# Kernel tuning notes

Measured on AMD Instinct MI355X. Metric: run time of the kernel, lower is better.

Reference implementation:

```python
import jax, jax.numpy as jnp
import numpy as np
from jax import lax

N, T, D, W, H, V = 256, 64, 1280, 256, 512, 10000
NULL_IDX = 0  # ignore_index


def setup_inputs() -> dict:
    key = jax.random.key(0)
    ks = jax.random.split(key, 9)
    features = jax.random.normal(ks[0], (N, D), dtype=jnp.float32)
    captions = jax.random.randint(ks[1], (N, T + 1), 0, V, dtype=jnp.int64)
    # learned parameters
    W_proj = jax.random.normal(ks[2], (D, H), dtype=jnp.float32) / np.sqrt(D)
    b_proj = jnp.zeros((H,), dtype=jnp.float32)
    W_embed = jax.random.normal(ks[3], (V, W), dtype=jnp.float32) / np.sqrt(V)
    Wx = jax.random.normal(ks[4], (W, H), dtype=jnp.float32) / np.sqrt(W)
    Wh = jax.random.normal(ks[5], (H, H), dtype=jnp.float32) / np.sqrt(H)
    b = jnp.zeros((H,), dtype=jnp.float32)
    W_out = jax.random.normal(ks[6], (H, V), dtype=jnp.float32) / np.sqrt(H)
    b_out = jnp.zeros((V,), dtype=jnp.float32)
    return {"features": features, "captions": captions, "W_proj": W_proj,
            "b_proj": b_proj, "W_embed": W_embed, "Wx": Wx, "Wh": Wh, "b": b,
            "W_out": W_out, "b_out": b_out}


def reference(features, captions, W_proj, b_proj, W_embed, Wx, Wh, b, W_out, b_out):
    captions_in = captions[:, :-1]   # (N, T)
    captions_out = captions[:, 1:]   # (N, T)

    h0 = features @ W_proj + b_proj                      # (N, H)
    x = W_embed[captions_in]                             # (N, T, W)
    # Precompute input-to-hidden part; recurrence only needs h @ Wh.
    xWxb = jnp.einsum('ntw,wh->nth', x, Wx) + b          # (N, T, H)

    def step(h_prev, xt):
        h_next = jnp.tanh(h_prev @ Wh + xt)
        return h_next, h_next

    _, hs = lax.scan(step, h0, jnp.swapaxes(xWxb, 0, 1))  # (T, N, H)
    h = jnp.swapaxes(hs, 0, 1)                            # (N, T, H)

    scores = jnp.einsum('nth,hv->ntv', h, W_out) + b_out  # (N, T, V)
    logp = jax.nn.log_softmax(scores, axis=-1)
    nll = -jnp.take_along_axis(logp, captions_out[..., None], axis=-1)[..., 0]
    mask = (captions_out != NULL_IDX).astype(nll.dtype)
    loss = jnp.sum(nll * mask) / N
    return loss
```

## Files before the change

kernel.cpp:

```cpp
#include <hip/hip_runtime.h>
#include <hip/hip_bf16.h>
#include <hip/hip_fp8.h>

#define NB 256
#define TT 64
#define DD 1280
#define WW 256
#define HH 512
#define VV 10000
#define VP 10112
#define NCT 79
#define MROWS (NB*TT)

typedef short short8 __attribute__((ext_vector_type(8)));
typedef float f32x4 __attribute__((ext_vector_type(4)));
typedef int   int4v __attribute__((ext_vector_type(4)));
typedef int   int8v __attribute__((ext_vector_type(8)));

static __device__ __forceinline__ unsigned short f2bf(float x){
    unsigned int u = __float_as_uint(x);
    unsigned int r = u + 0x7FFFu + ((u >> 16) & 1u);
    return (unsigned short)(r >> 16);
}
static __device__ __forceinline__ float bf2f(unsigned short u){
    return __uint_as_float(((unsigned int)u) << 16);
}
static __device__ __forceinline__ unsigned char f2f8(float x){
    __hip_fp8_e4m3 q(x);
    return (unsigned char)q.__x;
}
static __device__ __forceinline__ unsigned enc4(float x){
    unsigned s = (x < 0.f) ? 8u : 0u;
    float a = fabsf(x);
    unsigned m;
    if      (a < 0.25f) m = 0;
    else if (a < 0.75f) m = 1;
    else if (a < 1.25f) m = 2;
    else if (a < 1.75f) m = 3;
    else if (a < 2.5f)  m = 4;
    else if (a < 3.5f)  m = 5;
    else if (a < 5.0f)  m = 6;
    else                m = 7;
    return s | m;
}
static __device__ __forceinline__ void gload16b(const unsigned char* g, unsigned char* l){
    __builtin_amdgcn_global_load_lds(
        (const __attribute__((address_space(1))) void*)g,
        (__attribute__((address_space(3))) void*)l, 16, 0, 0);
}


__global__ __launch_bounds__(256) void k_prep(const float* __restrict__ W_proj,
                                              unsigned short* __restrict__ Wpb,
                                              const float* __restrict__ Wx,
                                              unsigned short* __restrict__ WxT,
                                              const float* __restrict__ Wh,
                                              unsigned char* __restrict__ WhT4,
                                              const float* __restrict__ W_out,
                                              unsigned char* __restrict__ WoT8p,
                                              const float* __restrict__ bo,
                                              float* __restrict__ bop){
    __shared__ unsigned short tileS[64][17];
    int b = blockIdx.x;
    int tid = threadIdx.x;
    if (b < 640){
        int i = b*256 + tid;
        float4 f = *reinterpret_cast<const float4*>(W_proj + (size_t)i*4);
        unsigned short* o = Wpb + (size_t)i*4;
        o[0]=f2bf(f.x); o[1]=f2bf(f.y); o[2]=f2bf(f.z); o[3]=f2bf(f.w);
    } else if (b < 768){
        int r = b - 640;
        int c0 = (r & 7)*64, r0 = (r >> 3)*16;
        int c = tid & 63, rr = tid >> 6;
        #pragma unroll
        for (int j = 0; j < 4; ++j){
            int rw_ = rr + j*4;
            tileS[c][rw_] = f2bf(Wx[(size_t)(r0+rw_)*HH + c0 + c]);
        }
        __syncthreads();
        int rw = tid & 15, cw = tid >> 4;
        #pragma unroll
        for (int j = 0; j < 4; ++j){
            int c2 = cw + j*16;
            WxT[(size_t)(c0+c2)*WW + r0 + rw] = tileS[c2][rw];
        }
    } else if (b < 1280){
        int r = b - 768;
        int j = r >> 1;
        int col = (r & 1)*256 + tid;
        float w0 = Wh[(size_t)(2*j  )*HH + col] * 32.0f;
        float w1 = Wh[(size_t)(2*j+1)*HH + col] * 32.0f;
        WhT4[(size_t)col*256 + j] = (unsigned char)(enc4(w0) | (enc4(w1) << 4));
    } else if (b < 6336){
        unsigned char (*tileC)[20] = reinterpret_cast<unsigned char (*)[20]>(&tileS[0][0]);
        int r = b - 1280;
        int c0 = (r % 158)*64, r0 = (r / 158)*16;
        int c = tid & 63, rr = tid >> 6;
        #pragma unroll
        for (int j = 0; j < 4; ++j){
            int rw_ = rr + j*4;
            unsigned char v = 0;
            if (c0 + c < VV) v = f2f8(W_out[(size_t)(r0+rw_)*VV + c0 + c]);
            tileC[c][rw_] = v;
        }
        __syncthreads();
        int rw = tid & 15, cw = tid >> 4;
        #pragma unroll
        for (int j = 0; j < 4; ++j){
            int c2 = cw + j*16;
            int col = c0 + c2, k = r0 + rw;
            if (col < VP){
                size_t addr = ((size_t)((col >> 7)*4 + (k >> 7)))*16384
                            + (unsigned)((col & 127)*128 + (k & 127));
                WoT8p[addr] = tileC[c2][rw];
            }
        }
    } else {
        int i = (b - 6336)*256 + tid;
        if (i < VP) bop[i] = (i < VV) ? bo[i] : -30000.0f;
    }
}

__global__ __launch_bounds__(512) void k_h0(const float* __restrict__ feat,
                                            const unsigned short* __restrict__ Wpb,
                                            const float* __restrict__ bp,
                                            float* __restrict__ h0){
    int n0 = blockIdx.x*2;
    int h = threadIdx.x;
    const float* f0 = feat + (size_t)(n0+0)*DD;
    const float* f1 = feat + (size_t)(n0+1)*DD;
    float a0=0.f, a1=0.f;
    for (int d = 0; d < DD; d += 4){
        #pragma unroll
        for (int j = 0; j < 4; ++j){
            float w = bf2f(Wpb[(size_t)(d+j)*HH + h]);
            a0 += f0[d+j]*w;
            a1 += f1[d+j]*w;
        }
    }
    float bb = bp[h];
    h0[(size_t)(n0+0)*HH+h] = a0+bb;
    h0[(size_t)(n0+1)*HH+h] = a1+bb;
}

__global__ __launch_bounds__(256) void k_e2(const float* __restrict__ We,
                                            const unsigned short* __restrict__ WxT,
                                            const float* __restrict__ bias,
                                            unsigned short* __restrict__ E2b){
    int lane = threadIdx.x & 63;
    int wv   = threadIdx.x >> 6;
    int l15 = lane & 15, lhi = lane >> 4;
    int rbase = blockIdx.x*64 + wv*16;
    int arow = rbase + l15; if (arow > VV-1) arow = VV-1;
    short8 a[8];
    #pragma unroll
    for (int kk = 0; kk < 8; ++kk){
        const float* src = We + (size_t)arow*WW + kk*32 + lhi*8;
        float4 g0 = *reinterpret_cast<const float4*>(src);
        float4 g1 = *reinterpret_cast<const float4*>(src + 4);
        short8 v;
        v[0]=(short)f2bf(g0.x); v[1]=(short)f2bf(g0.y); v[2]=(short)f2bf(g0.z); v[3]=(short)f2bf(g0.w);
        v[4]=(short)f2bf(g1.x); v[5]=(short)f2bf(g1.y); v[6]=(short)f2bf(g1.z); v[7]=(short)f2bf(g1.w);
        a[kk] = v;
    }
    int ct0 = blockIdx.y*16;
    for (int ct = ct0; ct < ct0+16; ++ct){
        int c0 = ct*16;
        f32x4 acc = {0.f,0.f,0.f,0.f};
        #pragma unroll
        for (int kk = 0; kk < 8; ++kk){
            short8 b = *reinterpret_cast<const short8*>(WxT + (size_t)(c0 + l15)*WW + kk*32 + lhi*8);
            acc = __builtin_amdgcn_mfma_f32_16x16x32_bf16(a[kk], b, acc, 0, 0, 0);
        }
        float bb = bias[c0 + l15];
        #pragma unroll
        for (int r = 0; r < 4; ++r){
            int row = rbase + lhi*4 + r;
            if (row < VV) E2b[(size_t)row*HH + c0 + l15] = f2bf(acc[r] + bb);
        }
    }
}

__global__ __launch_bounds__(512, 2) void k_rnn(const float* __restrict__ h0,
                                                const unsigned char* __restrict__ WhT4,
                                                const unsigned short* __restrict__ E2b,
                                                const int* __restrict__ caps,
                                                unsigned char* __restrict__ hA8){
    __shared__ __align__(32) unsigned char hl[2][HH];
    int tid = threadIdx.x;
    int lane = tid & 63, wv = tid >> 6;
    int l15 = lane & 15, lhi = lane >> 4;
    int n = blockIdx.x;
    int c0w = wv*64;
    int mycol = c0w + lane;
    unsigned char* hbase = hA8 + ((size_t)((n>>1)*4 + (wv>>1)))*16384
                               + (unsigned)((n&1)*64*128 + (mycol & 127));

    int4v b[4][4];
    #pragma unroll
    for (int ct = 0; ct < 4; ++ct){
        int col = c0w + ct*16 + l15;
        #pragma unroll
        for (int kt = 0; kt < 4; ++kt){
            b[ct][kt] = *reinterpret_cast<const int4v*>(WhT4 + (size_t)col*256 + kt*64 + lhi*16);
            asm volatile("" : "+v"(b[ct][kt]));
        }
    }
    hl[0][tid] = f2f8(h0[(size_t)n*HH + tid]);
    __syncthreads();
    int cur = 0;
    for (int t = 0; t < TT; ++t){
        int tok = caps[n*(TT+1) + t];
        unsigned short xv = E2b[(size_t)tok*HH + mycol];
        int8v a[4];
        #pragma unroll
        for (int kt = 0; kt < 4; ++kt)
            a[kt] = *reinterpret_cast<const int8v*>(&hl[cur][kt*128 + lhi*32]);
        f32x4 acc[4];
        #pragma unroll
        for (int ct = 0; ct < 4; ++ct){
            acc[ct] = (f32x4){0.f,0.f,0.f,0.f};
            #pragma unroll
            for (int kt = 0; kt < 4; ++kt){
                int8v bb = __builtin_shufflevector(b[ct][kt], b[ct][kt], 0,1,2,3,0,1,2,3);
                acc[ct] = __builtin_amdgcn_mfma_scale_f32_16x16x128_f8f6f4(
                    a[kt], bb, acc[ct],
                    0, 4,
                    0, (int)0x7F7F7F7F,
                    0, (int)0x7A7A7A7A);
            }
        }
        float v = (lhi == 0) ? acc[0][0] : (lhi == 1) ? acc[1][0]
                : (lhi == 2) ? acc[2][0] : acc[3][0];
        float x = v + bf2f(xv);
        float e = __expf(2.f*x);
        float th = 1.f - 2.f/(e + 1.f);
        unsigned char hv = f2f8(th);
        hl[cur^1][mycol] = hv;
        hbase[t*128] = hv;
        __syncthreads();
        cur ^= 1;
    }
}

__global__ __launch_bounds__(256) void k_scores(const unsigned char* __restrict__ hA8,
                                                const unsigned char* __restrict__ WoT8p,
                                                const float* __restrict__ bop,
                                                const int* __restrict__ caps,
                                                float* __restrict__ pps,
                                                float* __restrict__ pts){
    __shared__ unsigned char As[2*16384];
    __shared__ unsigned char Bs[2*16384];
    int bid = blockIdx.x;
    int x = bid & 7;
    int local = bid >> 3;
    int ct = local >> 4;
    int rt = x*16 + (local & 15);

    int tid = threadIdx.x;
    int lane = tid & 63, wv = tid >> 6;
    int l15 = lane & 15, lhi = lane >> 4;
    int wr = wv >> 1, wc = wv & 1;
    const unsigned char* Abase = hA8   + (size_t)rt*65536;
    const unsigned char* Bbase = WoT8p + (size_t)ct*65536;

    unsigned coff[4];
    #pragma unroll
    for (int i = 0; i < 4; ++i){
        unsigned chunk = (unsigned)(i*256 + tid);
        unsigned rowloc = chunk >> 3;
        coff[i] = rowloc*128 + (((chunk & 7u) ^ (rowloc & 7u))*16u);
    }

    f32x4 acc[4][4];
    #pragma unroll
    for (int m = 0; m < 4; ++m)
        #pragma unroll
        for (int n = 0; n < 4; ++n)
            acc[m][n] = (f32x4){0.f,0.f,0.f,0.f};

    for (int kt2 = 0; kt2 < 2; ++kt2){
        #pragma unroll
        for (int s = 0; s < 2; ++s){
            int kt = kt2*2 + s;
            #pragma unroll
            for (int i = 0; i < 4; ++i){
                gload16b(Abase + kt*16384 + coff[i], As + s*16384 + (unsigned)((i*256 + wv*64)*16));
                gload16b(Bbase + kt*16384 + coff[i], Bs + s*16384 + (unsigned)((i*256 + wv*64)*16));
            }
        }
        __syncthreads();
        #pragma unroll
        for (int s = 0; s < 2; ++s){
            const unsigned char* Ak = As + s*16384;
            const unsigned char* Bk = Bs + s*16384;
            int8v af[4], bf[4];
            #pragma unroll
            for (int m = 0; m < 4; ++m){
                unsigned row = (unsigned)(wr*64 + m*16 + l15);
                int4v c0 = *reinterpret_cast<const int4v*>(Ak + row*128 + (((unsigned)(lhi*2+0) ^ (row&7))*16));
                int4v c1 = *reinterpret_cast<const int4v*>(Ak + row*128 + (((unsigned)(lhi*2+1) ^ (row&7))*16));
                af[m] = __builtin_shufflevector(c0, c1, 0,1,2,3,4,5,6,7);
            }
            #pragma unroll
            for (int n = 0; n < 4; ++n){
                unsigned col = (unsigned)(wc*64 + n*16 + l15);
                int4v c0 = *reinterpret_cast<const int4v*>(Bk + col*128 + (((unsigned)(lhi*2+0) ^ (col&7))*16));
                int4v c1 = *reinterpret_cast<const int4v*>(Bk + col*128 + (((unsigned)(lhi*2+1) ^ (col&7))*16));
                bf[n] = __builtin_shufflevector(c0, c1, 0,1,2,3,4,5,6,7);
            }
            #pragma unroll
            for (int m = 0; m < 4; ++m)
                #pragma unroll
                for (int n = 0; n < 4; ++n)
                    acc[m][n] = __builtin_amdgcn_mfma_scale_f32_16x16x128_f8f6f4(
                        af[m], bf[n], acc[m][n],
                        0, 0,
                        0, (int)0x7F7F7F7F,
                        0, (int)0x7F7F7F7F);
        }
        __syncthreads();
    }

    int tg[4][4];
    float srun[4][4], ts[4][4];
    #pragma unroll
    for (int m = 0; m < 4; ++m)
        #pragma unroll
        for (int r = 0; r < 4; ++r){
            int gr = rt*128 + wr*64 + m*16 + lhi*4 + r;
            tg[m][r] = caps[(gr >> 6)*(TT+1) + (gr & 63) + 1];
            srun[m][r] = 0.f; ts[m][r] = 0.f;
        }
    #pragma unroll
    for (int n = 0; n < 4; ++n){
        int colg = ct*128 + wc*64 + n*16 + l15;
        float bb = bop[colg];
        #pragma unroll
        for (int m = 0; m < 4; ++m)
            #pragma unroll
            for (int r = 0; r < 4; ++r){
                float sc = acc[m][n][r] + bb;
                srun[m][r] += __expf(sc);
                if (tg[m][r] == colg) ts[m][r] += sc;
            }
    }
    #pragma unroll
    for (int off = 1; off < 16; off <<= 1)
        #pragma unroll
        for (int m = 0; m < 4; ++m)
            #pragma unroll
            for (int r = 0; r < 4; ++r){
                srun[m][r] += __shfl_xor(srun[m][r], off, 64);
                ts[m][r]   += __shfl_xor(ts[m][r],   off, 64);
            }
    float* red = (float*)As;
    if (wc == 1 && l15 == 0){
        #pragma unroll
        for (int m = 0; m < 4; ++m)
            #pragma unroll
            for (int r = 0; r < 4; ++r){
                int ri = wr*64 + m*16 + lhi*4 + r;
                red[ri]       = srun[m][r];
                red[128 + ri] = ts[m][r];
            }
    }
    __syncthreads();
    if (wc == 0 && l15 == 0){
        #pragma unroll
        for (int m = 0; m < 4; ++m)
            #pragma unroll
            for (int r = 0; r < 4; ++r){
                int ri = wr*64 + m*16 + lhi*4 + r;
                int gr = rt*128 + ri;
                pps[(size_t)ct*MROWS + gr] = srun[m][r] + red[ri];
                pts[(size_t)ct*MROWS + gr] = ts[m][r]   + red[128 + ri];
            }
    }
}

__global__ __launch_bounds__(256) void k_loss1(const float* __restrict__ pps,
                                               const float* __restrict__ pts,
                                               const int* __restrict__ caps,
                                               float* __restrict__ bsum){
    __shared__ float reds[256], redt[256];
    int tid = threadIdx.x;
    int rloc = tid & 63, q = tid >> 6;
    int row = blockIdx.x*64 + rloc;
    int c0 = q*20, c1 = (q == 3) ? NCT : c0 + 20;
    float s = 0.f, t0 = 0.f;
    for (int ct = c0; ct < c1; ++ct){
        s  += pps[(size_t)ct*MROWS + row];
        t0 += pts[(size_t)ct*MROWS + row];
    }
    reds[tid] = s; redt[tid] = t0;
    __syncthreads();
    if (q == 0){
        s  = reds[rloc] + reds[64+rloc] + reds[128+rloc] + reds[192+rloc];
        t0 = redt[rloc] + redt[64+rloc] + redt[128+rloc] + redt[192+rloc];
        int tgt = caps[(row >> 6)*(TT+1) + (row & 63) + 1];
        reds[rloc] = (tgt != 0) ? (__logf(s) - t0) : 0.f;
    }
    __syncthreads();
    if (tid < 32) reds[tid] += reds[tid+32];
    __syncthreads();
    if (tid < 16) reds[tid] += reds[tid+16];
    __syncthreads();
    if (tid < 8)  reds[tid] += reds[tid+8];
    __syncthreads();
    if (tid < 4)  reds[tid] += reds[tid+4];
    __syncthreads();
    if (tid == 0) bsum[blockIdx.x] = reds[0] + reds[1] + reds[2] + reds[3];
}

__global__ __launch_bounds__(64) void k_loss2(const float* __restrict__ bsum, float* __restrict__ out){
    __shared__ float red[64];
    int tid = threadIdx.x;
    red[tid] = bsum[tid] + bsum[tid+64] + bsum[tid+128] + bsum[tid+192];
    __syncthreads();
    for (int off = 32; off > 0; off >>= 1){
        if (tid < off) red[tid] += red[tid+off];
        __syncthreads();
    }
    if (tid == 0) out[0] = red[0] / (float)NB;
}

extern "C" void kernel_launch(void* const* d_in, const int* in_sizes, int n_in,
                              void* d_out, int out_size, void* d_ws, size_t ws_size,
                              hipStream_t stream) {
    const float* features = (const float*)d_in[0];
    const int*   captions = (const int*)  d_in[1];
    const float* W_proj   = (const float*)d_in[2];
    const float* b_proj   = (const float*)d_in[3];
    const float* W_embed  = (const float*)d_in[4];
    const float* Wx       = (const float*)d_in[5];
    const float* Wh       = (const float*)d_in[6];
    const float* b_       = (const float*)d_in[7];
    const float* W_out    = (const float*)d_in[8];
    const float* b_out    = (const float*)d_in[9];
    float* out = (float*)d_out;

    char* ws = (char*)d_ws;
    unsigned short* E2b   = (unsigned short*)(ws + 0);
    float*          h0    = (float*)         (ws + 10240000);
    unsigned char*  WhT4  = (unsigned char*) (ws + 10764288);
    unsigned short* WxT   = (unsigned short*)(ws + 10895360);
    unsigned char*  WoT8p = (unsigned char*) (ws + 11157504);
    float*          bop   = (float*)         (ws + 16334848);
    unsigned char*  hA8   = (unsigned char*) (ws + 16375296);
    float*          pps   = (float*)         (ws + 24763904);
    float*          pts   = (float*)         (ws + 29941248);
    float*          bsum  = (float*)         (ws + 35118592);
    unsigned short* Wpb   = (unsigned short*)(ws + 35119616);
    if (ws_size < 36430336u) return;

    k_prep<<<6376, 256, 0, stream>>>(W_proj, Wpb, Wx, WxT, Wh, WhT4, W_out, WoT8p, b_out, bop);
    k_h0<<<NB/2, 512, 0, stream>>>(features, Wpb, b_proj, h0);
    k_e2<<<dim3(157,2), 256, 0, stream>>>(W_embed, WxT, b_, E2b);
    k_rnn<<<NB, 512, 0, stream>>>(h0, WhT4, E2b, captions, hA8);
    k_scores<<<128*NCT, 256, 0, stream>>>(hA8, WoT8p, bop, captions, pps, pts);
    k_loss1<<<256, 256, 0, stream>>>(pps, pts, captions, bsum);
    k_loss2<<<1, 64, 0, stream>>>(bsum, out);
}
```

Baseline: 326.2 us.

## Use 512-thread blocks in scores GEMM with single-buffered K tiles

The scores kernel now runs 8 waves per 128x128 tile instead of 4. Each wave computes a 32x64 sub-tile, which halves the accumulator registers per thread. Shared staging shrinks from two K slices to one, and the K loop becomes four load-sync-compute iterations. This trades fewer registers and LDS per block (higher occupancy) for more barriers and less load batching per sync.

Result: no change. 323.0 us (-1.0%).

```diff
diff --git a/kernel.cpp b/kernel.cpp
--- a/kernel.cpp
+++ b/kernel.cpp
@@ -243,14 +243,14 @@
     }
 }
 
-__global__ __launch_bounds__(256) void k_scores(const unsigned char* __restrict__ hA8,
+__global__ __launch_bounds__(512) void k_scores(const unsigned char* __restrict__ hA8,
                                                 const unsigned char* __restrict__ WoT8p,
                                                 const float* __restrict__ bop,
                                                 const int* __restrict__ caps,
                                                 float* __restrict__ pps,
                                                 float* __restrict__ pts){
-    __shared__ unsigned char As[2*16384];
-    __shared__ unsigned char Bs[2*16384];
+    __shared__ unsigned char As[16384];
+    __shared__ unsigned char Bs[16384];
     int bid = blockIdx.x;
     int x = bid & 7;
     int local = bid >> 3;
@@ -264,71 +264,60 @@
     const unsigned char* Abase = hA8   + (size_t)rt*65536;
     const unsigned char* Bbase = WoT8p + (size_t)ct*65536;
 
-    unsigned coff[4];
-    #pragma unroll
-    for (int i = 0; i < 4; ++i){
-        unsigned chunk = (unsigned)(i*256 + tid);
+    unsigned coff[2];
+    #pragma unroll
+    for (int i = 0; i < 2; ++i){
+        unsigned chunk = (unsigned)(i*512 + tid);
         unsigned rowloc = chunk >> 3;
         coff[i] = rowloc*128 + (((chunk & 7u) ^ (rowloc & 7u))*16u);
     }
 
-    f32x4 acc[4][4];
-    #pragma unroll
-    for (int m = 0; m < 4; ++m)
+    f32x4 acc[2][4];
+    #pragma unroll
+    for (int m = 0; m < 2; ++m)
         #pragma unroll
         for (int n = 0; n < 4; ++n)
             acc[m][n] = (f32x4){0.f,0.f,0.f,0.f};
 
-    for (int kt2 = 0; kt2 < 2; ++kt2){
-        #pragma unroll
-        for (int s = 0; s < 2; ++s){
-            int kt = kt2*2 + s;
-            #pragma unroll
-            for (int i = 0; i < 4; ++i){
-                gload16b(Abase + kt*16384 + coff[i], As + s*16384 + (unsigned)((i*256 + wv*64)*16));
-                gload16b(Bbase + kt*16384 + coff[i], Bs + s*16384 + (unsigned)((i*256 + wv*64)*16));
-            }
-        }
-        __syncthreads();
-        #pragma unroll
-        for (int s = 0; s < 2; ++s){
-            const unsigned char* Ak = As + s*16384;
-            const unsigned char* Bk = Bs + s*16384;
-            int8v af[4], bf[4];
-            #pragma unroll
-            for (int m = 0; m < 4; ++m){
-                unsigned row = (unsigned)(wr*64 + m*16 + l15);
-                int4v c0 = *reinterpret_cast<const int4v*>(Ak + row*128 + (((unsigned)(lhi*2+0) ^ (row&7))*16));
-                int4v c1 = *reinterpret_cast<const int4v*>(Ak + row*128 + (((unsigned)(lhi*2+1) ^ (row&7))*16));
-                af[m] = __builtin_shufflevector(c0, c1, 0,1,2,3,4,5,6,7);
-            }
-            #pragma unroll
-            for (int n = 0; n < 4; ++n){
-                unsigned col = (unsigned)(wc*64 + n*16 + l15);
-                int4v c0 = *reinterpret_cast<const int4v*>(Bk + col*128 + (((unsigned)(lhi*2+0) ^ (col&7))*16));
-                int4v c1 = *reinterpret_cast<const int4v*>(Bk + col*128 + (((unsigned)(lhi*2+1) ^ (col&7))*16));
-                bf[n] = __builtin_shufflevector(c0, c1, 0,1,2,3,4,5,6,7);
-            }
-            #pragma unroll
-            for (int m = 0; m < 4; ++m)
-                #pragma unroll
-                for (int n = 0; n < 4; ++n)
-                    acc[m][n] = __builtin_amdgcn_mfma_scale_f32_16x16x128_f8f6f4(
-                        af[m], bf[n], acc[m][n],
-                        0, 0,
-                        0, (int)0x7F7F7F7F,
-                        0, (int)0x7F7F7F7F);
-        }
-        __syncthreads();
-    }
-
-    int tg[4][4];
-    float srun[4][4], ts[4][4];
-    #pragma unroll
-    for (int m = 0; m < 4; ++m)
+    for (int kt = 0; kt < 4; ++kt){
+        #pragma unroll
+        for (int i = 0; i < 2; ++i){
+            gload16b(Abase + kt*16384 + coff[i], As + (unsigned)((i*512 + tid - lane + lane) * 16));
+            gload16b(Bbase + kt*16384 + coff[i], Bs + (unsigned)((i*512 + tid) * 16));
+        }
+        __syncthreads();
+        int8v af[2];
+        #pragma unroll
+        for (int m = 0; m < 2; ++m){
+            unsigned row = (unsigned)(wr*32 + m*16 + l15);
+            int4v c0 = *reinterpret_cast<const int4v*>(As + row*128 + (((unsigned)(lhi*2+0) ^ (row&7))*16));
+            int4v c1 = *reinterpret_cast<const int4v*>(As + row*128 + (((unsigned)(lhi*2+1) ^ (row&7))*16));
+            af[m] = __builtin_shufflevector(c0, c1, 0,1,2,3,4,5,6,7);
+        }
+        #pragma unroll
+        for (int n = 0; n < 4; ++n){
+            unsigned col = (unsigned)(wc*64 + n*16 + l15);
+            int4v c0 = *reinterpret_cast<const int4v*>(Bs + col*128 + (((unsigned)(lhi*2+0) ^ (col&7))*16));
+            int4v c1 = *reinterpret_cast<const int4v*>(Bs + col*128 + (((unsigned)(lhi*2+1) ^ (col&7))*16));
+            int8v bf = __builtin_shufflevector(c0, c1, 0,1,2,3,4,5,6,7);
+            #pragma unroll
+            for (int m = 0; m < 2; ++m)
+                acc[m][n] = __builtin_amdgcn_mfma_scale_f32_16x16x128_f8f6f4(
+                    af[m], bf, acc[m][n],
+                    0, 0,
+                    0, (int)0x7F7F7F7F,
+                    0, (int)0x7F7F7F7F);
+        }
+        __syncthreads();
+    }
+
+    int tg[2][4];
+    float srun[2][4], ts[2][4];
+    #pragma unroll
+    for (int m = 0; m < 2; ++m)
         #pragma unroll
         for (int r = 0; r < 4; ++r){
-            int gr = rt*128 + wr*64 + m*16 + lhi*4 + r;
+            int gr = rt*128 + wr*32 + m*16 + lhi*4 + r;
             tg[m][r] = caps[(gr >> 6)*(TT+1) + (gr & 63) + 1];
             srun[m][r] = 0.f; ts[m][r] = 0.f;
         }
@@ -337,7 +326,7 @@
         int colg = ct*128 + wc*64 + n*16 + l15;
         float bb = bop[colg];
         #pragma unroll
-        for (int m = 0; m < 4; ++m)
+        for (int m = 0; m < 2; ++m)
             #pragma unroll
             for (int r = 0; r < 4; ++r){
                 float sc = acc[m][n][r] + bb;
@@ -348,7 +337,7 @@
     #pragma unroll
     for (int off = 1; off < 16; off <<= 1)
         #pragma unroll
-        for (int m = 0; m < 4; ++m)
+        for (int m = 0; m < 2; ++m)
             #pragma unroll
             for (int r = 0; r < 4; ++r){
                 srun[m][r] += __shfl_xor(srun[m][r], off, 64);
@@ -357,10 +346,10 @@
     float* red = (float*)As;
     if (wc == 1 && l15 == 0){
         #pragma unroll
-        for (int m = 0; m < 4; ++m)
+        for (int m = 0; m < 2; ++m)
             #pragma unroll
             for (int r = 0; r < 4; ++r){
-                int ri = wr*64 + m*16 + lhi*4 + r;
+                int ri = wr*32 + m*16 + lhi*4 + r;
                 red[ri]       = srun[m][r];
                 red[128 + ri] = ts[m][r];
             }
@@ -368,10 +357,10 @@
     __syncthreads();
     if (wc == 0 && l15 == 0){
         #pragma unroll
-        for (int m = 0; m < 4; ++m)
+        for (int m = 0; m < 2; ++m)
             #pragma unroll
             for (int r = 0; r < 4; ++r){
-                int ri = wr*64 + m*16 + lhi*4 + r;
+                int ri = wr*32 + m*16 + lhi*4 + r;
                 int gr = rt*128 + ri;
                 pps[(size_t)ct*MROWS + gr] = srun[m][r] + red[ri];
                 pts[(size_t)ct*MROWS + gr] = ts[m][r]   + red[128 + ri];
@@ -458,7 +447,7 @@
     k_h0<<<NB/2, 512, 0, stream>>>(features, Wpb, b_proj, h0);
     k_e2<<<dim3(157,2), 256, 0, stream>>>(W_embed, WxT, b_, E2b);
     k_rnn<<<NB, 512, 0, stream>>>(h0, WhT4, E2b, captions, hA8);
-    k_scores<<<128*NCT, 256, 0, stream>>>(hA8, WoT8p, bop, captions, pps, pts);
+    k_scores<<<128*NCT, 512, 0, stream>>>(hA8, WoT8p, bop, captions, pps, pts);
     k_loss1<<<256, 256, 0, stream>>>(pps, pts, captions, bsum);
     k_loss2<<<1, 64, 0, stream>>>(bsum, out);
 }
```
